# Kernel optimization log

Measured on AMD Instinct MI355X. Metric: run time of the kernel, lower is better.

The kernel has to match this reference:

```python
import jax, jax.numpy as jnp
import numpy as np

N_NODES = 50000


def sage_conv(x, edge_index, w_l, w_r, b):
    # PyG SAGEConv (aggr='mean', root_weight=True):
    #   out = mean_{j in N(i)} x_j @ w_l + x_i @ w_r + b
    src = edge_index[0]  # message source j
    dst = edge_index[1]  # message target i
    msgs = x[src]                                        # [E, C_in] gather
    agg = jax.ops.segment_sum(msgs, dst, num_segments=N_NODES)   # [N, C_in]
    deg = jax.ops.segment_sum(jnp.ones((src.shape[0],), x.dtype), dst,
                              num_segments=N_NODES)              # [N]
    agg = agg / jnp.maximum(deg, 1.0)[:, None]           # mean aggregation
    return agg @ w_l + x @ w_r + b


def setup_inputs() -> dict:
    key = jax.random.key(0)
    ks = jax.random.split(key, 8)
    in_c, hid_c, out_c = 96, 128, 64
    x = jax.random.normal(ks[0], (N_NODES, in_c), dtype=jnp.float32)
    edge_index = jax.random.randint(ks[1], (2, 800000), 0, N_NODES, dtype=jnp.int64)
    def glorot(k, fan_in, fan_out):
        lim = float(np.sqrt(6.0 / (fan_in + fan_out)))
        return jax.random.uniform(k, (fan_in, fan_out), jnp.float32, -lim, lim)
    return {
        'x': x,
        'edge_index': edge_index,
        'w1_l': glorot(ks[2], in_c, hid_c),
        'w1_r': glorot(ks[3], in_c, hid_c),
        'b1': jnp.zeros((hid_c,), jnp.float32),
        'w2_l': glorot(ks[4], hid_c, out_c),
        'w2_r': glorot(ks[5], hid_c, out_c),
        'b2': jnp.zeros((out_c,), jnp.float32),
    }


def reference(x, edge_index, w1_l, w1_r, b1, w2_l, w2_r, b2):
    h = sage_conv(x, edge_index, w1_l, w1_r, b1)
    h = jax.nn.relu(h)
    out = sage_conv(h, edge_index, w2_l, w2_r, b2)
    return out
```

## Files before the change

### kernel.cpp

```cpp
#include <hip/hip_runtime.h>
#include <hip/hip_bf16.h>

#define N_NODES 50000
#define IN_C    96
#define HID_C   128
#define OUT_C   64
#define MROWS   50016

#define NB      200
#define BSZ     250
#define WCHUNK  4096
#define NWG     196

#define XBLKS   2344
#define WBLKS   160

typedef __attribute__((ext_vector_type(8))) short short8;
typedef __attribute__((ext_vector_type(4))) float f32x4;

__device__ inline unsigned int f2bf(float f) {
    unsigned int u = __float_as_uint(f);
    return (u + 0x7fffu + ((u >> 16) & 1u)) >> 16;
}
__device__ inline unsigned int pack2(float lo, float hi) {
    return f2bf(lo) | (f2bf(hi) << 16);
}
__device__ inline float blo(unsigned int u) { return __uint_as_float(u << 16); }
__device__ inline float bhi(unsigned int u) { return __uint_as_float(u & 0xffff0000u); }

__global__ __launch_bounds__(256) void parta_hist(
    const int* __restrict__ dst, int* __restrict__ gh, int E)
{
    __shared__ int h[NB];
    int t = threadIdx.x;
    if (t < NB) h[t] = 0;
    __syncthreads();
    int base_e = blockIdx.x * WCHUNK;
    for (int i = t; i < WCHUNK; i += 256) {
        int e = base_e + i;
        if (e < E) atomicAdd(&h[dst[e] / BSZ], 1);
    }
    __syncthreads();
    if (t < NB) gh[blockIdx.x * NB + t] = h[t];
}

__global__ __launch_bounds__(256) void parta_scan(
    const int* __restrict__ gh, int* __restrict__ ofs,
    int* __restrict__ base)
{
    __shared__ int buf[256];
    int t = threadIdx.x;
    int tot = 0;
    if (t < NB) {
        for (int w = 0; w < NWG; w++) tot += gh[w * NB + t];
    }
    buf[t] = tot;
    __syncthreads();
    for (int off = 1; off < 256; off <<= 1) {
        int v = (t >= off) ? buf[t - off] : 0;
        __syncthreads();
        buf[t] += v;
        __syncthreads();
    }
    if (t < NB) {
        int excl = buf[t] - tot;
        base[t] = excl;
        if (t == NB - 1) base[NB] = excl + tot;
        int run = excl;
        for (int w = 0; w < NWG; w++) {
            ofs[w * NB + t] = run;
            run += gh[w * NB + t];
        }
    }
}

__global__ __launch_bounds__(256) void parta_scatter(
    const int* __restrict__ src, const int* __restrict__ dst,
    const int* __restrict__ ofs, uint2* __restrict__ pairs, int E)
{
    __shared__ int cur[NB];
    int t = threadIdx.x;
    if (t < NB) cur[t] = ofs[blockIdx.x * NB + t];
    __syncthreads();
    int base_e = blockIdx.x * WCHUNK;
    for (int i = t; i < WCHUNK; i += 256) {
        int e = base_e + i;
        if (e < E) {
            int d = dst[e];
            int pos = atomicAdd(&cur[d / BSZ], 1);
            pairs[pos] = make_uint2((unsigned)src[e], (unsigned)d);
        }
    }
}

__global__ __launch_bounds__(256) void partb_csr(
    const uint2* __restrict__ pairs, const int* __restrict__ base,
    int* __restrict__ rowstart, int* __restrict__ cnt,
    int* __restrict__ adj)
{
    __shared__ int h[256];
    __shared__ int buf[256];
    __shared__ int cur[256];
    int b = blockIdx.x;
    int t = threadIdx.x;
    int beg = base[b], end = base[b + 1];
    int node0 = b * BSZ;
    h[t] = 0;
    __syncthreads();
    for (int i = beg + t; i < end; i += 256)
        atomicAdd(&h[(int)pairs[i].y - node0], 1);
    __syncthreads();
    int c = h[t];
    buf[t] = c;
    __syncthreads();
    for (int off = 1; off < 256; off <<= 1) {
        int v = (t >= off) ? buf[t - off] : 0;
        __syncthreads();
        buf[t] += v;
        __syncthreads();
    }
    int excl = buf[t] - c;
    if (t < BSZ) {
        rowstart[node0 + t] = beg + excl;
        cnt[node0 + t] = c;
    }
    cur[t] = beg + excl;
    __syncthreads();
    for (int i = beg + t; i < end; i += 256) {
        uint2 pr = pairs[i];
        int pos = atomicAdd(&cur[(int)pr.y - node0], 1);
        adj[pos] = (int)pr.x;
    }
}

__global__ __launch_bounds__(256) void conv_all_kernel(
    const float* __restrict__ x, uint4* __restrict__ xb4,
    const float* __restrict__ w1l, const float* __restrict__ w1r,
    const float* __restrict__ w2l, const float* __restrict__ w2r,
    unsigned short* __restrict__ wt1, unsigned short* __restrict__ wt2)
{
    int blk = blockIdx.x;
    if (blk < XBLKS) {
        int idx = blk * 256 + threadIdx.x;
        if (idx >= N_NODES * 12) return;
        const float4* x4 = (const float4*)x;
        float4 u = x4[(size_t)idx * 2];
        float4 v = x4[(size_t)idx * 2 + 1];
        uint4 w;
        w.x = pack2(u.x, u.y); w.y = pack2(u.z, u.w);
        w.z = pack2(v.x, v.y); w.w = pack2(v.z, v.w);
        xb4[idx] = w;
    } else {
        int i = (blk - XBLKS) * 256 + threadIdx.x;
        if (i < 128 * 192) {
            int col = i / 192, k = i - col * 192;
            float v = (k < 96) ? w1l[k * 128 + col] : w1r[(k - 96) * 128 + col];
            wt1[i] = (unsigned short)f2bf(v);
        } else {
            int j = i - 128 * 192;
            int col = j / 128, k = j - col * 128;
            float v = (col < 64) ? w2l[k * 64 + col] : w2r[k * 64 + col - 64];
            wt2[j] = (unsigned short)f2bf(v);
        }
    }
}

__global__ __launch_bounds__(256) void gather1_kernel(
    const int* __restrict__ rowstart, const int* __restrict__ cnt,
    const int* __restrict__ adj, const uint4* __restrict__ xb4,
    uint4* __restrict__ agg4)
{
    int idx = blockIdx.x * 256 + threadIdx.x;
    if (idx >= N_NODES * 12) return;
    int node = idx / 12;
    int c = idx - node * 12;
    int beg = rowstart[node];
    int d = cnt[node];
    int end = beg + d;
    float a0=0,a1=0,a2=0,a3=0,a4=0,a5=0,a6=0,a7=0;
    float b0=0,b1=0,b2=0,b3=0,b4=0,b5=0,b6=0,b7=0;
    int j = beg;
    for (; j + 3 < end; j += 4) {
        int s0 = adj[j];
        int s1 = adj[j + 1];
        int s2 = adj[j + 2];
        int s3 = adj[j + 3];
        uint4 u = xb4[(size_t)s0 * 12 + c];
        uint4 v = xb4[(size_t)s1 * 12 + c];
        uint4 w = xb4[(size_t)s2 * 12 + c];
        uint4 z = xb4[(size_t)s3 * 12 + c];
        a0 += blo(u.x); a1 += bhi(u.x); a2 += blo(u.y); a3 += bhi(u.y);
        a4 += blo(u.z); a5 += bhi(u.z); a6 += blo(u.w); a7 += bhi(u.w);
        b0 += blo(v.x); b1 += bhi(v.x); b2 += blo(v.y); b3 += bhi(v.y);
        b4 += blo(v.z); b5 += bhi(v.z); b6 += blo(v.w); b7 += bhi(v.w);
        a0 += blo(w.x); a1 += bhi(w.x); a2 += blo(w.y); a3 += bhi(w.y);
        a4 += blo(w.z); a5 += bhi(w.z); a6 += blo(w.w); a7 += bhi(w.w);
        b0 += blo(z.x); b1 += bhi(z.x); b2 += blo(z.y); b3 += bhi(z.y);
        b4 += blo(z.z); b5 += bhi(z.z); b6 += blo(z.w); b7 += bhi(z.w);
    }
    for (; j < end; j++) {
        int s0 = adj[j];
        uint4 u = xb4[(size_t)s0 * 12 + c];
        a0 += blo(u.x); a1 += bhi(u.x); a2 += blo(u.y); a3 += bhi(u.y);
        a4 += blo(u.z); a5 += bhi(u.z); a6 += blo(u.w); a7 += bhi(u.w);
    }
    a0 += b0; a1 += b1; a2 += b2; a3 += b3;
    a4 += b4; a5 += b5; a6 += b6; a7 += b7;
    float id = 1.0f / (float)max(d, 1);
    uint4 w;
    w.x = pack2(a0 * id, a1 * id); w.y = pack2(a2 * id, a3 * id);
    w.z = pack2(a4 * id, a5 * id); w.w = pack2(a6 * id, a7 * id);
    agg4[(size_t)node * 12 + c] = w;
}

__global__ __launch_bounds__(256) void gemm1_mfma(
    const uint4* __restrict__ agg4, const uint4* __restrict__ xb4,
    const uint4* __restrict__ w4,
    const float* __restrict__ b1, unsigned short* __restrict__ h)
{
    constexpr int KD = 192, KP = KD + 8;
    __shared__ unsigned short lw[128 * KP];
    __shared__ unsigned short la[32 * KP];
    int t = threadIdx.x;
    uint4* lw4 = (uint4*)lw;
    uint4* la4 = (uint4*)la;
    for (int i = t; i < 128 * 24; i += 256) {
        int r = i / 24, c = i - r * 24;
        lw4[r * 25 + c] = w4[i];
    }
    int row0 = blockIdx.x * 32;
    for (int i = t; i < 32 * 24; i += 256) {
        int r = i / 24, c = i - r * 24;
        la4[r * 25 + c] = (c < 12)
            ? agg4[(size_t)(row0 + r) * 12 + c]
            : xb4[(size_t)(row0 + r) * 12 + (c - 12)];
    }
    __syncthreads();

    int wave = t >> 6, lane = t & 63;
    int m = lane & 15, half = lane >> 4;
    int koff = half * 8;
    f32x4 acc00 = {}, acc01 = {}, acc10 = {}, acc11 = {};
#pragma unroll
    for (int k0 = 0; k0 < KD; k0 += 32) {
        short8 A0 = *(const short8*)&la[(m)      * KP + k0 + koff];
        short8 A1 = *(const short8*)&la[(16 + m) * KP + k0 + koff];
        short8 B0 = *(const short8*)&lw[(wave * 32 + m)      * KP + k0 + koff];
        short8 B1 = *(const short8*)&lw[(wave * 32 + 16 + m) * KP + k0 + koff];
        acc00 = __builtin_amdgcn_mfma_f32_16x16x32_bf16(A0, B0, acc00, 0, 0, 0);
        acc01 = __builtin_amdgcn_mfma_f32_16x16x32_bf16(A0, B1, acc01, 0, 0, 0);
        acc10 = __builtin_amdgcn_mfma_f32_16x16x32_bf16(A1, B0, acc10, 0, 0, 0);
        acc11 = __builtin_amdgcn_mfma_f32_16x16x32_bf16(A1, B1, acc11, 0, 0, 0);
    }
    int col0 = wave * 32 + m;
    int col1 = wave * 32 + 16 + m;
    float bias0 = b1[col0], bias1 = b1[col1];
#pragma unroll
    for (int reg = 0; reg < 4; reg++) {
        int r0 = row0 + half * 4 + reg;
        int r1 = r0 + 16;
        if (r0 < N_NODES) {
            h[(size_t)r0 * 128 + col0] = (unsigned short)f2bf(fmaxf(acc00[reg] + bias0, 0.f));
            h[(size_t)r0 * 128 + col1] = (unsigned short)f2bf(fmaxf(acc01[reg] + bias1, 0.f));
        }
        if (r1 < N_NODES) {
            h[(size_t)r1 * 128 + col0] = (unsigned short)f2bf(fmaxf(acc10[reg] + bias0, 0.f));
            h[(size_t)r1 * 128 + col1] = (unsigned short)f2bf(fmaxf(acc11[reg] + bias1, 0.f));
        }
    }
}

__global__ __launch_bounds__(256) void gemm2_mfma(
    const uint4* __restrict__ h4, const uint4* __restrict__ w4,
    const float* __restrict__ b2, unsigned short* __restrict__ p,
    float* __restrict__ out)
{
    constexpr int KD = 128, KP = KD + 8;
    __shared__ unsigned short lw[128 * KP];
    __shared__ unsigned short la[32 * KP];
    int t = threadIdx.x;
    uint4* lw4 = (uint4*)lw;
    uint4* la4 = (uint4*)la;
    for (int i = t; i < 128 * 16; i += 256) {
        int r = i >> 4, c = i & 15;
        lw4[r * 17 + c] = w4[i];
    }
    int row0 = blockIdx.x * 32;
    for (int i = t; i < 32 * 16; i += 256) {
        int r = i >> 4, c = i & 15;
        la4[r * 17 + c] = h4[(size_t)(row0 + r) * 16 + c];
    }
    __syncthreads();

    int wave = t >> 6, lane = t & 63;
    int m = lane & 15, half = lane >> 4;
    int koff = half * 8;
    f32x4 acc00 = {}, acc01 = {}, acc10 = {}, acc11 = {};
#pragma unroll
    for (int k0 = 0; k0 < KD; k0 += 32) {
        short8 A0 = *(const short8*)&la[(m)      * KP + k0 + koff];
        short8 A1 = *(const short8*)&la[(16 + m) * KP + k0 + koff];
        short8 B0 = *(const short8*)&lw[(wave * 32 + m)      * KP + k0 + koff];
        short8 B1 = *(const short8*)&lw[(wave * 32 + 16 + m) * KP + k0 + koff];
        acc00 = __builtin_amdgcn_mfma_f32_16x16x32_bf16(A0, B0, acc00, 0, 0, 0);
        acc01 = __builtin_amdgcn_mfma_f32_16x16x32_bf16(A0, B1, acc01, 0, 0, 0);
        acc10 = __builtin_amdgcn_mfma_f32_16x16x32_bf16(A1, B0, acc10, 0, 0, 0);
        acc11 = __builtin_amdgcn_mfma_f32_16x16x32_bf16(A1, B1, acc11, 0, 0, 0);
    }
    int col0 = wave * 32 + m;
    int col1 = wave * 32 + 16 + m;
#pragma unroll
    for (int reg = 0; reg < 4; reg++) {
        int r0 = row0 + half * 4 + reg;
        int r1 = r0 + 16;
        float v00 = acc00[reg], v01 = acc01[reg];
        float v10 = acc10[reg], v11 = acc11[reg];
        if (r0 < N_NODES) {
            if (col0 < 64) p[(size_t)r0 * 64 + col0] = (unsigned short)f2bf(v00);
            else           out[(size_t)r0 * 64 + col0 - 64] = v00 + b2[col0 - 64];
            if (col1 < 64) p[(size_t)r0 * 64 + col1] = (unsigned short)f2bf(v01);
            else           out[(size_t)r0 * 64 + col1 - 64] = v01 + b2[col1 - 64];
        }
        if (r1 < N_NODES) {
            if (col0 < 64) p[(size_t)r1 * 64 + col0] = (unsigned short)f2bf(v10);
            else           out[(size_t)r1 * 64 + col0 - 64] = v10 + b2[col0 - 64];
            if (col1 < 64) p[(size_t)r1 * 64 + col1] = (unsigned short)f2bf(v11);
            else           out[(size_t)r1 * 64 + col1 - 64] = v11 + b2[col1 - 64];
        }
    }
}

__global__ __launch_bounds__(256) void gather2_kernel(
    const int* __restrict__ rowstart, const int* __restrict__ cnt,
    const int* __restrict__ adj, const uint4* __restrict__ p4,
    float* __restrict__ out)
{
    int idx = blockIdx.x * 256 + threadIdx.x;
    if (idx >= N_NODES * 8) return;
    int node = idx >> 3;
    int c = idx & 7;
    int beg = rowstart[node];
    int d = cnt[node];
    int end = beg + d;
    float a0=0,a1=0,a2=0,a3=0,a4=0,a5=0,a6=0,a7=0;
    float b0=0,b1=0,b2=0,b3=0,b4=0,b5=0,b6=0,b7=0;
    int j = beg;
    for (; j + 3 < end; j += 4) {
        int s0 = adj[j];
        int s1 = adj[j + 1];
        int s2 = adj[j + 2];
        int s3 = adj[j + 3];
        uint4 u = p4[(size_t)s0 * 8 + c];
        uint4 v = p4[(size_t)s1 * 8 + c];
        uint4 w = p4[(size_t)s2 * 8 + c];
        uint4 z = p4[(size_t)s3 * 8 + c];
        a0 += blo(u.x); a1 += bhi(u.x); a2 += blo(u.y); a3 += bhi(u.y);
        a4 += blo(u.z); a5 += bhi(u.z); a6 += blo(u.w); a7 += bhi(u.w);
        b0 += blo(v.x); b1 += bhi(v.x); b2 += blo(v.y); b3 += bhi(v.y);
        b4 += blo(v.z); b5 += bhi(v.z); b6 += blo(v.w); b7 += bhi(v.w);
        a0 += blo(w.x); a1 += bhi(w.x); a2 += blo(w.y); a3 += bhi(w.y);
        a4 += blo(w.z); a5 += bhi(w.z); a6 += blo(w.w); a7 += bhi(w.w);
        b0 += blo(z.x); b1 += bhi(z.x); b2 += blo(z.y); b3 += bhi(z.y);
        b4 += blo(z.z); b5 += bhi(z.z); b6 += blo(z.w); b7 += bhi(z.w);
    }
    for (; j < end; j++) {
        int s0 = adj[j];
        uint4 u = p4[(size_t)s0 * 8 + c];
        a0 += blo(u.x); a1 += bhi(u.x); a2 += blo(u.y); a3 += bhi(u.y);
        a4 += blo(u.z); a5 += bhi(u.z); a6 += blo(u.w); a7 += bhi(u.w);
    }
    a0 += b0; a1 += b1; a2 += b2; a3 += b3;
    a4 += b4; a5 += b5; a6 += b6; a7 += b7;
    float id = 1.0f / (float)max(d, 1);
    float4* o4 = (float4*)out;
    size_t base = (size_t)node * 16 + 2 * c;
    float4 u = o4[base], v = o4[base + 1];
    u.x = fmaf(a0, id, u.x); u.y = fmaf(a1, id, u.y);
    u.z = fmaf(a2, id, u.z); u.w = fmaf(a3, id, u.w);
    v.x = fmaf(a4, id, v.x); v.y = fmaf(a5, id, v.y);
    v.z = fmaf(a6, id, v.z); v.w = fmaf(a7, id, v.w);
    o4[base] = u; o4[base + 1] = v;
}

extern "C" void kernel_launch(void* const* d_in, const int* in_sizes, int n_in,
                              void* d_out, int out_size, void* d_ws, size_t ws_size,
                              hipStream_t stream)
{
    const float* x   = (const float*)d_in[0];
    const int*   ei  = (const int*)d_in[1];
    const float* w1l = (const float*)d_in[2];
    const float* w1r = (const float*)d_in[3];
    const float* b1  = (const float*)d_in[4];
    const float* w2l = (const float*)d_in[5];
    const float* w2r = (const float*)d_in[6];
    const float* b2  = (const float*)d_in[7];
    float* out = (float*)d_out;

    int E = in_sizes[1] / 2;
    const int* src = ei;
    const int* dst = ei + E;

    int* gh       = (int*)d_ws;
    int* ofs      = gh + NWG * NB;
    int* base     = ofs + NWG * NB;
    int* cnt      = base + 256;
    int* rowstart = cnt + N_NODES;
    uint2* pairs  = (uint2*)(rowstart + N_NODES);
    int* adj      = (int*)(pairs + 800000);
    unsigned short* xb  = (unsigned short*)(adj + 800000);
    unsigned short* agg = xb + (size_t)N_NODES * IN_C;
    unsigned short* h   = agg + (size_t)MROWS * 96;
    unsigned short* p   = h  + (size_t)MROWS * 128;
    unsigned short* Wt1 = p  + (size_t)N_NODES * 64;
    unsigned short* Wt2 = Wt1 + 128 * 192;

    parta_hist<<<NWG, 256, 0, stream>>>(dst, gh, E);
    parta_scan<<<1, 256, 0, stream>>>(gh, ofs, base);
    parta_scatter<<<NWG, 256, 0, stream>>>(src, dst, ofs, pairs, E);
    partb_csr<<<NB, 256, 0, stream>>>(pairs, base, rowstart, cnt, adj);

    conv_all_kernel<<<XBLKS + WBLKS, 256, 0, stream>>>(
        x, (uint4*)xb, w1l, w1r, w2l, w2r, Wt1, Wt2);

    gather1_kernel<<<(N_NODES * 12 + 255) / 256, 256, 0, stream>>>(
        rowstart, cnt, adj, (const uint4*)xb, (uint4*)agg);

    gemm1_mfma<<<MROWS / 32, 256, 0, stream>>>(
        (const uint4*)agg, (const uint4*)xb, (const uint4*)Wt1, b1, h);
    gemm2_mfma<<<MROWS / 32, 256, 0, stream>>>(
        (const uint4*)h, (const uint4*)Wt2, b2, p, out);

    gather2_kernel<<<(N_NODES * 8 + 255) / 256, 256, 0, stream>>>(
        rowstart, cnt, adj, (const uint4*)p, out);
}
```

Measured before the change: 201.1 us.

## Fuse layer-1 and layer-2 GEMMs via LDS-resident hidden tile; retune histogram chunking

Merges the two MFMA GEMM kernels into one. The layer-1 output tile h (64 rows) stays in LDS and feeds the layer-2 GEMM directly, so h is never written to or reread from global memory and one launch goes away. Row tiles grow from 32 to 64 to amortize weight loads, which lowers the block count and raises LDS use. The partition histogram also moves to fewer, larger chunks (NWG 49, WCHUNK 16384), and the buffers are re-laid out with MROWS padding for the larger tile.

```diff
diff --git a/kernel.cpp b/kernel.cpp
--- a/kernel.cpp
+++ b/kernel.cpp
@@ -5,12 +5,12 @@
 #define IN_C    96
 #define HID_C   128
 #define OUT_C   64
-#define MROWS   50016
+#define MROWS   50048
 
 #define NB      200
 #define BSZ     250
-#define WCHUNK  4096
-#define NWG     196
+#define WCHUNK  16384
+#define NWG     49
 
 #define XBLKS   2344
 #define WBLKS   160
@@ -213,23 +213,26 @@
     agg4[(size_t)node * 12 + c] = w;
 }
 
-__global__ __launch_bounds__(256) void gemm1_mfma(
+__global__ __launch_bounds__(256) void gemm12_fused(
     const uint4* __restrict__ agg4, const uint4* __restrict__ xb4,
-    const uint4* __restrict__ w4,
-    const float* __restrict__ b1, unsigned short* __restrict__ h)
-{
-    constexpr int KD = 192, KP = KD + 8;
+    const uint4* __restrict__ w1t4, const uint4* __restrict__ w2t4,
+    const float* __restrict__ b1, const float* __restrict__ b2,
+    unsigned short* __restrict__ p, float* __restrict__ out)
+{
+    constexpr int KP = 200;
+    constexpr int KQ = 136;
     __shared__ unsigned short lw[128 * KP];
-    __shared__ unsigned short la[32 * KP];
+    __shared__ unsigned short la[64 * KP];
     int t = threadIdx.x;
     uint4* lw4 = (uint4*)lw;
     uint4* la4 = (uint4*)la;
+
     for (int i = t; i < 128 * 24; i += 256) {
         int r = i / 24, c = i - r * 24;
-        lw4[r * 25 + c] = w4[i];
-    }
-    int row0 = blockIdx.x * 32;
-    for (int i = t; i < 32 * 24; i += 256) {
+        lw4[r * 25 + c] = w1t4[i];
+    }
+    int row0 = blockIdx.x * 64;
+    for (int i = t; i < 64 * 24; i += 256) {
         int r = i / 24, c = i - r * 24;
         la4[r * 25 + c] = (c < 12)
             ? agg4[(size_t)(row0 + r) * 12 + c]
@@ -240,92 +243,62 @@
     int wave = t >> 6, lane = t & 63;
     int m = lane & 15, half = lane >> 4;
     int koff = half * 8;
-    f32x4 acc00 = {}, acc01 = {}, acc10 = {}, acc11 = {};
-#pragma unroll
-    for (int k0 = 0; k0 < KD; k0 += 32) {
-        short8 A0 = *(const short8*)&la[(m)      * KP + k0 + koff];
-        short8 A1 = *(const short8*)&la[(16 + m) * KP + k0 + koff];
+    f32x4 acc[4][2] = {};
+#pragma unroll
+    for (int k0 = 0; k0 < 192; k0 += 32) {
         short8 B0 = *(const short8*)&lw[(wave * 32 + m)      * KP + k0 + koff];
         short8 B1 = *(const short8*)&lw[(wave * 32 + 16 + m) * KP + k0 + koff];
-        acc00 = __builtin_amdgcn_mfma_f32_16x16x32_bf16(A0, B0, acc00, 0, 0, 0);
-        acc01 = __builtin_amdgcn_mfma_f32_16x16x32_bf16(A0, B1, acc01, 0, 0, 0);
-        acc10 = __builtin_amdgcn_mfma_f32_16x16x32_bf16(A1, B0, acc10, 0, 0, 0);
-        acc11 = __builtin_amdgcn_mfma_f32_16x16x32_bf16(A1, B1, acc11, 0, 0, 0);
-    }
-    int col0 = wave * 32 + m;
-    int col1 = wave * 32 + 16 + m;
-    float bias0 = b1[col0], bias1 = b1[col1];
-#pragma unroll
-    for (int reg = 0; reg < 4; reg++) {
-        int r0 = row0 + half * 4 + reg;
-        int r1 = r0 + 16;
-        if (r0 < N_NODES) {
-            h[(size_t)r0 * 128 + col0] = (unsigned short)f2bf(fmaxf(acc00[reg] + bias0, 0.f));
-            h[(size_t)r0 * 128 + col1] = (unsigned short)f2bf(fmaxf(acc01[reg] + bias1, 0.f));
-        }
-        if (r1 < N_NODES) {
-            h[(size_t)r1 * 128 + col0] = (unsigned short)f2bf(fmaxf(acc10[reg] + bias0, 0.f));
-            h[(size_t)r1 * 128 + col1] = (unsigned short)f2bf(fmaxf(acc11[reg] + bias1, 0.f));
-        }
-    }
-}
-
-__global__ __launch_bounds__(256) void gemm2_mfma(
-    const uint4* __restrict__ h4, const uint4* __restrict__ w4,
-    const float* __restrict__ b2, unsigned short* __restrict__ p,
-    float* __restrict__ out)
-{
-    constexpr int KD = 128, KP = KD + 8;
-    __shared__ unsigned short lw[128 * KP];
-    __shared__ unsigned short la[32 * KP];
-    int t = threadIdx.x;
-    uint4* lw4 = (uint4*)lw;
-    uint4* la4 = (uint4*)la;
+#pragma unroll
+        for (int g = 0; g < 4; g++) {
+            short8 A = *(const short8*)&la[(g * 16 + m) * KP + k0 + koff];
+            acc[g][0] = __builtin_amdgcn_mfma_f32_16x16x32_bf16(A, B0, acc[g][0], 0, 0, 0);
+            acc[g][1] = __builtin_amdgcn_mfma_f32_16x16x32_bf16(A, B1, acc[g][1], 0, 0, 0);
+        }
+    }
+    __syncthreads();
+
+    int col0 = wave * 32 + m, col1 = col0 + 16;
+    {
+        float bias0 = b1[col0], bias1 = b1[col1];
+#pragma unroll
+        for (int g = 0; g < 4; g++) {
+#pragma unroll
+            for (int reg = 0; reg < 4; reg++) {
+                int hr = g * 16 + half * 4 + reg;
+                la[hr * KQ + col0] = (unsigned short)f2bf(fmaxf(acc[g][0][reg] + bias0, 0.f));
+                la[hr * KQ + col1] = (unsigned short)f2bf(fmaxf(acc[g][1][reg] + bias1, 0.f));
+            }
+        }
+    }
     for (int i = t; i < 128 * 16; i += 256) {
         int r = i >> 4, c = i & 15;
-        lw4[r * 17 + c] = w4[i];
-    }
-    int row0 = blockIdx.x * 32;
-    for (int i = t; i < 32 * 16; i += 256) {
-        int r = i >> 4, c = i & 15;
-        la4[r * 17 + c] = h4[(size_t)(row0 + r) * 16 + c];
-    }
-    __syncthreads();
-
-    int wave = t >> 6, lane = t & 63;
-    int m = lane & 15, half = lane >> 4;
-    int koff = half * 8;
-    f32x4 acc00 = {}, acc01 = {}, acc10 = {}, acc11 = {};
-#pragma unroll
-    for (int k0 = 0; k0 < KD; k0 += 32) {
-        short8 A0 = *(const short8*)&la[(m)      * KP + k0 + koff];
-        short8 A1 = *(const short8*)&la[(16 + m) * KP + k0 + koff];
-        short8 B0 = *(const short8*)&lw[(wave * 32 + m)      * KP + k0 + koff];
-        short8 B1 = *(const short8*)&lw[(wave * 32 + 16 + m) * KP + k0 + koff];
-        acc00 = __builtin_amdgcn_mfma_f32_16x16x32_bf16(A0, B0, acc00, 0, 0, 0);
-        acc01 = __builtin_amdgcn_mfma_f32_16x16x32_bf16(A0, B1, acc01, 0, 0, 0);
-        acc10 = __builtin_amdgcn_mfma_f32_16x16x32_bf16(A1, B0, acc10, 0, 0, 0);
-        acc11 = __builtin_amdgcn_mfma_f32_16x16x32_bf16(A1, B1, acc11, 0, 0, 0);
-    }
-    int col0 = wave * 32 + m;
-    int col1 = wave * 32 + 16 + m;
-#pragma unroll
-    for (int reg = 0; reg < 4; reg++) {
-        int r0 = row0 + half * 4 + reg;
-        int r1 = r0 + 16;
-        float v00 = acc00[reg], v01 = acc01[reg];
-        float v10 = acc10[reg], v11 = acc11[reg];
-        if (r0 < N_NODES) {
-            if (col0 < 64) p[(size_t)r0 * 64 + col0] = (unsigned short)f2bf(v00);
-            else           out[(size_t)r0 * 64 + col0 - 64] = v00 + b2[col0 - 64];
-            if (col1 < 64) p[(size_t)r0 * 64 + col1] = (unsigned short)f2bf(v01);
-            else           out[(size_t)r0 * 64 + col1 - 64] = v01 + b2[col1 - 64];
-        }
-        if (r1 < N_NODES) {
-            if (col0 < 64) p[(size_t)r1 * 64 + col0] = (unsigned short)f2bf(v10);
-            else           out[(size_t)r1 * 64 + col0 - 64] = v10 + b2[col0 - 64];
-            if (col1 < 64) p[(size_t)r1 * 64 + col1] = (unsigned short)f2bf(v11);
-            else           out[(size_t)r1 * 64 + col1 - 64] = v11 + b2[col1 - 64];
+        lw4[r * 17 + c] = w2t4[i];
+    }
+    __syncthreads();
+
+    f32x4 acc2[4][2] = {};
+#pragma unroll
+    for (int k0 = 0; k0 < 128; k0 += 32) {
+        short8 B0 = *(const short8*)&lw[(wave * 32 + m)      * KQ + k0 + koff];
+        short8 B1 = *(const short8*)&lw[(wave * 32 + 16 + m) * KQ + k0 + koff];
+#pragma unroll
+        for (int g = 0; g < 4; g++) {
+            short8 A = *(const short8*)&la[(g * 16 + m) * KQ + k0 + koff];
+            acc2[g][0] = __builtin_amdgcn_mfma_f32_16x16x32_bf16(A, B0, acc2[g][0], 0, 0, 0);
+            acc2[g][1] = __builtin_amdgcn_mfma_f32_16x16x32_bf16(A, B1, acc2[g][1], 0, 0, 0);
+        }
+    }
+#pragma unroll
+    for (int g = 0; g < 4; g++) {
+#pragma unroll
+        for (int reg = 0; reg < 4; reg++) {
+            int r = row0 + g * 16 + half * 4 + reg;
+            if (r >= N_NODES) continue;
+            float v0 = acc2[g][0][reg], v1 = acc2[g][1][reg];
+            if (col0 < 64) p[(size_t)r * 64 + col0] = (unsigned short)f2bf(v0);
+            else           out[(size_t)r * 64 + col0 - 64] = v0 + b2[col0 - 64];
+            if (col1 < 64) p[(size_t)r * 64 + col1] = (unsigned short)f2bf(v1);
+            else           out[(size_t)r * 64 + col1 - 64] = v1 + b2[col1 - 64];
         }
     }
 }
@@ -408,9 +381,8 @@
     uint2* pairs  = (uint2*)(rowstart + N_NODES);
     int* adj      = (int*)(pairs + 800000);
     unsigned short* xb  = (unsigned short*)(adj + 800000);
-    unsigned short* agg = xb + (size_t)N_NODES * IN_C;
-    unsigned short* h   = agg + (size_t)MROWS * 96;
-    unsigned short* p   = h  + (size_t)MROWS * 128;
+    unsigned short* agg = xb + (size_t)MROWS * IN_C;
+    unsigned short* p   = agg + (size_t)MROWS * IN_C;
     unsigned short* Wt1 = p  + (size_t)N_NODES * 64;
     unsigned short* Wt2 = Wt1 + 128 * 192;
 
@@ -425,10 +397,9 @@
     gather1_kernel<<<(N_NODES * 12 + 255) / 256, 256, 0, stream>>>(
         rowstart, cnt, adj, (const uint4*)xb, (uint4*)agg);
 
-    gemm1_mfma<<<MROWS / 32, 256, 0, stream>>>(
-        (const uint4*)agg, (const uint4*)xb, (const uint4*)Wt1, b1, h);
-    gemm2_mfma<<<MROWS / 32, 256, 0, stream>>>(
-        (const uint4*)h, (const uint4*)Wt2, b2, p, out);
+    gemm12_fused<<<MROWS / 64, 256, 0, stream>>>(
+        (const uint4*)agg, (const uint4*)xb, (const uint4*)Wt1, (const uint4*)Wt2,
+        b1, b2, p, out);
 
     gather2_kernel<<<(N_NODES * 8 + 255) / 256, 256, 0, stream>>>(
         rowstart, cnt, adj, (const uint4*)p, out);
```

After: 229.4 us. 1.14x slower.
